# Performance work log

Hardware: AMD Instinct MI355X
Metric: run time of the kernel (lower is better)

Reference implementation:

```python
import jax, jax.numpy as jnp
import numpy as np

N, E, G, D, OUT, VOCAB = 100000, 1600000, 512, 128, 10, 500
BN_EPS = 1e-5


def _lin(h, W, b):
    return h @ W + b


def _mlp(h, W1, b1, W2, b2):
    return _lin(jax.nn.relu(_lin(h, W1, b1)), W2, b2)


def _bn(h, g, b):
    mu = jnp.mean(h, axis=0)
    var = jnp.var(h, axis=0)
    return (h - mu) * jax.lax.rsqrt(var + BN_EPS) * g + b


def setup_inputs() -> dict:
    key = jax.random.key(0)
    ks = jax.random.split(key, 32)
    s = 1.0 / np.sqrt(D)
    inp = {
        'x': jax.random.randint(ks[0], (N,), 0, VOCAB, dtype=jnp.int32),
        'edge_index': jax.random.randint(ks[1], (2, E), 0, N, dtype=jnp.int32),
        'batch': jnp.sort(jax.random.randint(ks[2], (N,), 0, G, dtype=jnp.int32)),
        'emb': jax.random.normal(ks[3], (VOCAB, D), jnp.float32),
        'iw1': jax.random.normal(ks[4], (D, D), jnp.float32) * s,
        'ib1': jnp.zeros((D,), jnp.float32),
        'iw2': jax.random.normal(ks[5], (D, D), jnp.float32) * s,
        'ib2': jnp.zeros((D,), jnp.float32),
        'f1w': jax.random.normal(ks[6], (D, D), jnp.float32) * s,
        'f1b': jnp.zeros((D,), jnp.float32),
        'f2w': jax.random.normal(ks[7], (D, OUT), jnp.float32) * s,
        'f2b': jnp.zeros((OUT,), jnp.float32),
    }
    for i, base in zip(range(3), (8, 14, 20)):
        l = i + 1
        inp[f'c{l}w1'] = jax.random.normal(ks[base], (D, D), jnp.float32) * s
        inp[f'c{l}b1'] = jnp.zeros((D,), jnp.float32)
        inp[f'c{l}w2'] = jax.random.normal(ks[base + 1], (D, D), jnp.float32) * s
        inp[f'c{l}b2'] = jnp.zeros((D,), jnp.float32)
        inp[f'g{l}'] = jnp.ones((D,), jnp.float32)
        inp[f'be{l}'] = jnp.zeros((D,), jnp.float32)
    return inp


def reference(x, edge_index, batch,
              emb, iw1, ib1, iw2, ib2,
              c1w1, c1b1, c1w2, c1b2, g1, be1,
              c2w1, c2b1, c2w2, c2b2, g2, be2,
              c3w1, c3b1, c3w2, c3b2, g3, be3,
              f1w, f1b, f2w, f2b):
    src, dst = edge_index[0], edge_index[1]

    def gin_conv(h, W1, b1, W2, b2):
        # scatter-add neighbor aggregation, eps = 0 -> (1+0)*x + sum_j x_j
        agg = jax.ops.segment_sum(h[src], dst, num_segments=N)
        return _mlp(h + agg, W1, b1, W2, b2)

    h = emb[x]                                   # [N, D] embedding lookup
    h = _mlp(h, iw1, ib1, iw2, ib2)              # initial_mlp
    h = jax.nn.relu(_bn(gin_conv(h, c1w1, c1b1, c1w2, c1b2), g1, be1))
    h = jax.nn.relu(_bn(gin_conv(h, c2w1, c2b1, c2w2, c2b2), g2, be2))
    h = jax.nn.relu(_bn(gin_conv(h, c3w1, c3b1, c3w2, c3b2), g3, be3))
    p = jax.ops.segment_sum(h, batch, num_segments=G)   # global_add_pool [G, D]
    p = jax.nn.relu(_lin(p, f1w, f1b))
    # dropout in eval mode = identity
    return _lin(p, f2w, f2b)                     # [G, OUT]
```

## Files before the change

kernel.cpp:

```cpp
#include <hip/hip_runtime.h>

typedef unsigned short u16;
typedef unsigned int u32;
typedef __bf16 bf16x8 __attribute__((ext_vector_type(8)));
typedef float f32x4 __attribute__((ext_vector_type(4)));

#define MFMA_BF16(a, b, c) __builtin_amdgcn_mfma_f32_16x16x32_bf16(a, b, c, 0, 0, 0)

#define NBUC_MAX 512
#define BCAP 4608
#define EPB 8192

__device__ __forceinline__ float bf2f(u16 h) {
  u32 u = ((u32)h) << 16;
  return __builtin_bit_cast(float, u);
}
__device__ __forceinline__ u16 f2bf(float f) {
  u32 u = __builtin_bit_cast(u32, f);
  u += 0x7fffu + ((u >> 16) & 1u);
  return (u16)(u >> 16);
}

__global__ __launch_bounds__(256) void prep_w6(const float* __restrict__ w0,
                                               const float* __restrict__ w1,
                                               const float* __restrict__ w2,
                                               const float* __restrict__ w3,
                                               const float* __restrict__ w4,
                                               const float* __restrict__ w5,
                                               u16* __restrict__ wt) {
  const int which = blockIdx.x >> 6;
  const float* w = which == 0 ? w0 : which == 1 ? w1 : which == 2 ? w2
                  : which == 3 ? w3 : which == 4 ? w4 : w5;
  int t = (blockIdx.x & 63) * 256 + threadIdx.x;
  int n = t >> 7, k = t & 127;
  wt[which * 16384 + n * 128 + k] = f2bf(w[k * 128 + n]);
}

__global__ __launch_bounds__(128) void mlp0_table(
    const float* __restrict__ emb, const float* __restrict__ w1, const float* __restrict__ b1,
    const float* __restrict__ w2, const float* __restrict__ b2, u16* __restrict__ table) {
  __shared__ float e[128];
  __shared__ float tt[128];
  int r = blockIdx.x, j = threadIdx.x;
  e[j] = emb[r * 128 + j];
  __syncthreads();
  float s = b1[j];
  for (int k = 0; k < 128; ++k) s += e[k] * w1[k * 128 + j];
  tt[j] = s > 0.f ? s : 0.f;
  __syncthreads();
  float s2 = b2[j];
  for (int k = 0; k < 128; ++k) s2 += tt[k] * w2[k * 128 + j];
  table[r * 128 + j] = f2bf(s2);
}

__global__ __launch_bounds__(256) void bucket_scatter(const int* __restrict__ src,
                                                      const int* __restrict__ dst,
                                                      u32* __restrict__ pairs,
                                                      u32* __restrict__ cursor, int E_, int nbuc) {
  __shared__ u32 sv[EPB];
  __shared__ u16 sb[EPB];
  __shared__ u32 lcnt[NBUC_MAX];
  __shared__ u32 lbase[NBUC_MAX];
  const int t = threadIdx.x;
  for (int b = t; b < NBUC_MAX; b += 256) lcnt[b] = 0;
  __syncthreads();
  const int e0 = blockIdx.x * EPB;
#pragma unroll
  for (int it = 0; it < EPB / 256; ++it) {
    int idx = it * 256 + t;
    int e = e0 + idx;
    u32 v = 0u;
    u16 b = 0xffffu;
    if (e < E_) {
      int s = src[e], d = dst[e];
      b = (u16)(d >> 8);
      v = ((u32)s << 8) | (u32)(d & 255);
      atomicAdd(&lcnt[b], 1u);
    }
    sv[idx] = v;
    sb[idx] = b;
  }
  __syncthreads();
  for (int b = t; b < nbuc; b += 256) {
    u32 c = lcnt[b];
    lbase[b] = c ? atomicAdd(&cursor[b], c) : 0u;
    lcnt[b] = 0;
  }
  __syncthreads();
#pragma unroll
  for (int it = 0; it < EPB / 256; ++it) {
    int idx = it * 256 + t;
    u16 b = sb[idx];
    if (b != 0xffffu) {
      u32 r = atomicAdd(&lcnt[b], 1u);
      u32 p = lbase[b] + r;
      if (p < BCAP) pairs[(size_t)b * BCAP + p] = sv[idx];
    }
  }
}

__global__ __launch_bounds__(256) void csr_build(const u32* __restrict__ pairs,
                                                 const u32* __restrict__ cursor,
                                                 u32* __restrict__ csr, int* __restrict__ RS,
                                                 int* __restrict__ DEG, int nrows) {
  __shared__ u32 cnt[256];
  __shared__ u32 offs[256];
  __shared__ u32 basearr[256];
  const int b = blockIdx.x, t = threadIdx.x;
  u32 count = cursor[b];
  if (count > BCAP) count = BCAP;
  cnt[t] = 0;
  __syncthreads();
  const u32* pb = pairs + (size_t)b * BCAP;
  for (u32 i = t; i < count; i += 256) atomicAdd(&cnt[pb[i] & 255u], 1u);
  __syncthreads();
  const u32 my = cnt[t];
  offs[t] = my;
  __syncthreads();
  for (int d = 1; d < 256; d <<= 1) {
    u32 v = (t >= d) ? offs[t - d] : 0u;
    __syncthreads();
    offs[t] += v;
    __syncthreads();
  }
  const u32 excl = offs[t] - my;
  const int node = (b << 8) + t;
  if (node < nrows) {
    RS[node] = b * BCAP + (int)excl;
    DEG[node] = (int)my;
  }
  basearr[t] = excl;
  cnt[t] = 0;
  __syncthreads();
  for (u32 i = t; i < count; i += 256) {
    u32 v = pb[i];
    u32 dl = v & 255u;
    u32 r = atomicAdd(&cnt[dl], 1u);
    csr[(size_t)b * BCAP + basearr[dl] + r] = v >> 8;
  }
}

template <int MODE>
__global__ __launch_bounds__(256) void agg_kernel(
    const u16* __restrict__ Hsrc, const int* __restrict__ x, const u32* __restrict__ csr,
    const int* __restrict__ RS, const int* __restrict__ DEG, const float* __restrict__ scsh,
    u16* __restrict__ AGG, int nrows) {
  int node = blockIdx.x * 4 + (threadIdx.x >> 6);
  if (node >= nrows) return;
  const int lane = threadIdx.x & 63;
  const int grp = lane >> 4;
  const int fl = lane & 15;
  const int deg = DEG[node];
  const u32* cl = csr + RS[node];
  const char* Hb = (const char*)Hsrc;
  const u32 flo = (u32)fl << 4;

  float sc[8], sh[8];
  if (MODE == 1) {
#pragma unroll
    for (int i = 0; i < 8; ++i) {
      sc[i] = scsh[fl * 8 + i];
      sh[i] = scsh[128 + fl * 8 + i];
    }
  }
  float a[8];
#pragma unroll
  for (int i = 0; i < 8; ++i) a[i] = 0.f;

#define ACCUM(vv)                                   \
  {                                                 \
    const u16* p = (const u16*)&(vv);               \
    _Pragma("unroll") for (int i = 0; i < 8; ++i) { \
      float xv = bf2f(p[i]);                        \
      if (MODE == 1) {                              \
        xv = xv * sc[i] + sh[i];                    \
        xv = xv > 0.f ? xv : 0.f;                   \
      }                                             \
      a[i] += xv;                                   \
    }                                               \
  }
#define ROWOFF(idx) ((((u32)(MODE == 0 ? x[(idx)] : (idx))) << 8) + flo)

  if (grp == 0) {
    uint4 v = *(const uint4*)(Hb + ROWOFF(node));
    ACCUM(v);
  }
  int j = grp;
  int cA = (j < deg) ? (int)cl[j] : 0;
  int cB = (j + 4 < deg) ? (int)cl[j + 4] : 0;
  uint4 nv = make_uint4(0u, 0u, 0u, 0u);
  if (j < deg) nv = *(const uint4*)(Hb + ROWOFF(cA));
  while (j < deg) {
    uint4 cv = nv;
    int cn = cB;
    cB = (j + 8 < deg) ? (int)cl[j + 8] : 0;
    if (j + 4 < deg) nv = *(const uint4*)(Hb + ROWOFF(cn));
    ACCUM(cv);
    j += 4;
  }
#undef ROWOFF
#undef ACCUM

#pragma unroll
  for (int i = 0; i < 8; ++i) {
    a[i] += __shfl_xor(a[i], 16);
    a[i] += __shfl_xor(a[i], 32);
  }
  if (grp == 0) {
    u32 o[4];
#pragma unroll
    for (int i = 0; i < 4; ++i) o[i] = (u32)f2bf(a[2 * i]) | ((u32)f2bf(a[2 * i + 1]) << 16);
    *(uint4*)(AGG + (size_t)node * 128 + fl * 8) = *(uint4*)o;
  }
}

__global__ __launch_bounds__(256) void mlp_kernel(
    const u16* __restrict__ X, const u16* __restrict__ W1t, const float* __restrict__ b1,
    const u16* __restrict__ W2t, const float* __restrict__ b2, u16* __restrict__ Y,
    float* __restrict__ stats, int nrows) {
  __shared__ u16 Xs[64 * 136];
  __shared__ u16 Ts[64 * 136];
  const int t = threadIdx.x;
  const int row0 = blockIdx.x * 64;
  {
    const int seg = t & 15;
    const int rb = t >> 4;
#pragma unroll
    for (int p = 0; p < 4; ++p) {
      const int r = rb + p * 16;
      const int gr = row0 + r;
      uint4 v = make_uint4(0u, 0u, 0u, 0u);
      if (gr < nrows) v = *(const uint4*)(X + (size_t)gr * 128 + seg * 8);
      *(uint4*)(Xs + r * 136 + seg * 8) = v;
    }
  }
  __syncthreads();
  const int lane = t & 63;
  const int wave = t >> 6;
  const int n0 = wave * 32;
  const int nl = lane & 15;
  const int quad = lane >> 4;

  bf16x8 bw[2][4];
#pragma unroll
  for (int nt = 0; nt < 2; ++nt)
#pragma unroll
    for (int kk = 0; kk < 4; ++kk)
      bw[nt][kk] = *(const bf16x8*)(W1t + (size_t)(n0 + nt * 16 + nl) * 128 + kk * 32 + quad * 8);

  f32x4 acc[4][2];
#pragma unroll
  for (int mt = 0; mt < 4; ++mt) {
    acc[mt][0] = (f32x4)0.0f;
    acc[mt][1] = (f32x4)0.0f;
  }
#pragma unroll
  for (int kk = 0; kk < 4; ++kk) {
#pragma unroll
    for (int mt = 0; mt < 4; ++mt) {
      bf16x8 a = *(const bf16x8*)(Xs + (mt * 16 + nl) * 136 + kk * 32 + quad * 8);
      acc[mt][0] = MFMA_BF16(a, bw[0][kk], acc[mt][0]);
      acc[mt][1] = MFMA_BF16(a, bw[1][kk], acc[mt][1]);
    }
  }
#pragma unroll
  for (int nt = 0; nt < 2; ++nt) {
    const int n = n0 + nt * 16 + nl;
    const float bias = b1[n];
#pragma unroll
    for (int mt = 0; mt < 4; ++mt)
#pragma unroll
      for (int r = 0; r < 4; ++r) {
        float v = acc[mt][nt][r] + bias;
        v = v > 0.f ? v : 0.f;
        Ts[(mt * 16 + quad * 4 + r) * 136 + n] = f2bf(v);
      }
  }
  __syncthreads();
#pragma unroll
  for (int nt = 0; nt < 2; ++nt)
#pragma unroll
    for (int kk = 0; kk < 4; ++kk)
      bw[nt][kk] = *(const bf16x8*)(W2t + (size_t)(n0 + nt * 16 + nl) * 128 + kk * 32 + quad * 8);
#pragma unroll
  for (int mt = 0; mt < 4; ++mt) {
    acc[mt][0] = (f32x4)0.0f;
    acc[mt][1] = (f32x4)0.0f;
  }
#pragma unroll
  for (int kk = 0; kk < 4; ++kk) {
#pragma unroll
    for (int mt = 0; mt < 4; ++mt) {
      bf16x8 a = *(const bf16x8*)(Ts + (mt * 16 + nl) * 136 + kk * 32 + quad * 8);
      acc[mt][0] = MFMA_BF16(a, bw[0][kk], acc[mt][0]);
      acc[mt][1] = MFMA_BF16(a, bw[1][kk], acc[mt][1]);
    }
  }
  float ssum[2] = {0.f, 0.f}, ssq[2] = {0.f, 0.f};
#pragma unroll
  for (int nt = 0; nt < 2; ++nt) {
    const int n = n0 + nt * 16 + nl;
    const float bias = b2[n];
#pragma unroll
    for (int mt = 0; mt < 4; ++mt)
#pragma unroll
      for (int r = 0; r < 4; ++r) {
        const int row = row0 + mt * 16 + quad * 4 + r;
        float v = acc[mt][nt][r] + bias;
        if (row < nrows) {
          Y[(size_t)row * 128 + n] = f2bf(v);
          ssum[nt] += v;
          ssq[nt] += v * v;
        }
      }
  }
#pragma unroll
  for (int nt = 0; nt < 2; ++nt) {
    float s = ssum[nt], q = ssq[nt];
    s += __shfl_xor(s, 16);
    q += __shfl_xor(q, 16);
    s += __shfl_xor(s, 32);
    q += __shfl_xor(q, 32);
    if (quad == 0) {
      const int n = n0 + nt * 16 + nl;
      atomicAdd(&stats[n], s);
      atomicAdd(&stats[128 + n], q);
    }
  }
}

__global__ __launch_bounds__(128) void bn_finalize(const float* __restrict__ stats,
                                                   const float* __restrict__ g,
                                                   const float* __restrict__ be,
                                                   float* __restrict__ scsh, float invN) {
  int f = threadIdx.x;
  float mu = stats[f] * invN;
  float var = stats[128 + f] * invN - mu * mu;
  float rstd = rsqrtf(var + 1e-5f);
  float sc = rstd * g[f];
  scsh[f] = sc;
  scsh[128 + f] = be[f] - mu * sc;
}

__global__ __launch_bounds__(256) void pool_final(
    const u16* __restrict__ Hh, const int* __restrict__ batch, const float* __restrict__ scsh,
    const float* __restrict__ f1w, const float* __restrict__ f1b, const float* __restrict__ f2w,
    const float* __restrict__ f2b, float* __restrict__ out, int nrows) {
  __shared__ float red[16][128];
  __shared__ float pr[128];
  __shared__ float tt[128];
  const int gid = blockIdx.x, t = threadIdx.x;
  int l = 0, r = nrows;
  while (l < r) {
    int m = (l + r) >> 1;
    if (batch[m] < gid) l = m + 1; else r = m;
  }
  const int s0 = l;
  r = nrows;
  while (l < r) {
    int m = (l + r) >> 1;
    if (batch[m] < gid + 1) l = m + 1; else r = m;
  }
  const int s1 = l;
  const int fl = t & 15;
  const int grp = t >> 4;
  float sc[8], sh[8];
#pragma unroll
  for (int i = 0; i < 8; ++i) {
    sc[i] = scsh[fl * 8 + i];
    sh[i] = scsh[128 + fl * 8 + i];
  }
  float a[8];
#pragma unroll
  for (int i = 0; i < 8; ++i) a[i] = 0.f;
  for (int i = s0 + grp; i < s1; i += 16) {
    uint4 v = *(const uint4*)(Hh + (size_t)i * 128 + fl * 8);
    const u16* pp = (const u16*)&v;
#pragma unroll
    for (int k = 0; k < 8; ++k) {
      float xv = bf2f(pp[k]) * sc[k] + sh[k];
      a[k] += xv > 0.f ? xv : 0.f;
    }
  }
#pragma unroll
  for (int k = 0; k < 8; ++k) red[grp][fl * 8 + k] = a[k];
  __syncthreads();
  if (t < 128) {
    float s = 0.f;
#pragma unroll
    for (int gg2 = 0; gg2 < 16; ++gg2) s += red[gg2][t];
    pr[t] = s;
  }
  __syncthreads();
  if (t < 128) {
    float s = f1b[t];
    for (int k = 0; k < 128; ++k) s += pr[k] * f1w[k * 128 + t];
    tt[t] = s > 0.f ? s : 0.f;
  }
  __syncthreads();
  if (t < 10) {
    float s2 = f2b[t];
    for (int k = 0; k < 128; ++k) s2 += tt[k] * f2w[k * 10 + t];
    out[gid * 10 + t] = s2;
  }
}

extern "C" void kernel_launch(void* const* d_in, const int* in_sizes, int n_in, void* d_out,
                              int out_size, void* d_ws, size_t ws_size, hipStream_t stream) {
  const int* x = (const int*)d_in[0];
  const int* ei = (const int*)d_in[1];
  const int* batch = (const int*)d_in[2];
  const float* emb = (const float*)d_in[3];
  const float* iw1 = (const float*)d_in[4];
  const float* ib1 = (const float*)d_in[5];
  const float* iw2 = (const float*)d_in[6];
  const float* ib2 = (const float*)d_in[7];
  const float* f1w = (const float*)d_in[8];
  const float* f1b = (const float*)d_in[9];
  const float* f2w = (const float*)d_in[10];
  const float* f2b = (const float*)d_in[11];
  const float* cw1[3] = {(const float*)d_in[12], (const float*)d_in[18], (const float*)d_in[24]};
  const float* cb1[3] = {(const float*)d_in[13], (const float*)d_in[19], (const float*)d_in[25]};
  const float* cw2[3] = {(const float*)d_in[14], (const float*)d_in[20], (const float*)d_in[26]};
  const float* cb2[3] = {(const float*)d_in[15], (const float*)d_in[21], (const float*)d_in[27]};
  const float* gg[3] = {(const float*)d_in[16], (const float*)d_in[22], (const float*)d_in[28]};
  const float* bb[3] = {(const float*)d_in[17], (const float*)d_in[23], (const float*)d_in[29]};

  const int N_ = in_sizes[0];
  const int E_ = in_sizes[1] / 2;
  const int V_ = in_sizes[3] / 128;
  const int G_ = out_size / 10;
  const int NBUC = (N_ + 255) >> 8;
  const float invN = 1.0f / (float)N_;

  char* ws = (char*)d_ws;
  u16* H = (u16*)(ws + 0);
  u16* AGG = (u16*)(ws + 25600000);
  u32* PAIRS = (u32*)(ws + 51200000);
  u32* CSR = (u32*)(ws + 60637184);
  int* RS = (int*)(ws + 70074368);
  int* DEG = (int*)(ws + 70474368);
  u32* CUR = (u32*)(ws + 70874368);
  float* STATS = (float*)(ws + 70876416);
  float* SCSH = (float*)(ws + 70879488);
  u16* WT = (u16*)(ws + 70882560);
  u16* TBL = (u16*)(ws + 71079168);

  hipMemsetAsync(ws + 70874368, 0, 5120, stream);

  prep_w6<<<384, 256, 0, stream>>>(cw1[0], cw2[0], cw1[1], cw2[1], cw1[2], cw2[2], WT);
  mlp0_table<<<V_, 128, 0, stream>>>(emb, iw1, ib1, iw2, ib2, TBL);
  bucket_scatter<<<(E_ + EPB - 1) / EPB, 256, 0, stream>>>(ei, ei + E_, PAIRS, CUR, E_, NBUC);
  csr_build<<<NBUC, 256, 0, stream>>>(PAIRS, CUR, CSR, RS, DEG, N_);

  const int ablk = (N_ + 3) / 4;
  const int mblk = (N_ + 63) / 64;
  for (int l = 0; l < 3; ++l) {
    const u16* W1 = WT + (size_t)l * 32768;
    const u16* W2 = WT + (size_t)l * 32768 + 16384;
    if (l == 0)
      agg_kernel<0><<<ablk, 256, 0, stream>>>(TBL, x, CSR, RS, DEG, nullptr, AGG, N_);
    else
      agg_kernel<1><<<ablk, 256, 0, stream>>>(H, nullptr, CSR, RS, DEG, SCSH + (l - 1) * 256,
                                              AGG, N_);
    mlp_kernel<<<mblk, 256, 0, stream>>>(AGG, W1, cb1[l], W2, cb2[l], H, STATS + l * 256, N_);
    bn_finalize<<<1, 128, 0, stream>>>(STATS + l * 256, gg[l], bb[l], SCSH + l * 256, invN);
  }
  pool_final<<<G_, 256, 0, stream>>>(H, batch, SCSH + 2 * 256, f1w, f1b, f2w, f2b,
                                     (float*)d_out, N_);
}
```

Baseline: 543.3 us.

## Unfuse BN-apply from aggregation and drop LDS staging in bucket scatter

Batch-norm scale/shift plus ReLU is moved out of the gather loop into a separate bn_apply kernel that normalizes H in place once per layer, so the aggregation only converts and adds neighbor rows. The aim is to avoid redoing the affine and ReLU for every edge (about 16 times per node). The cost is an extra launch and a full read-write pass over H. Separately, bucket_scatter no longer stages src/dst in shared memory and re-reads them from global memory in the second pass, which frees LDS for higher occupancy at the cost of a second read of the edge list.

New measurement: 570.5 us. +5.0%, slower.

```diff
diff --git a/kernel.cpp b/kernel.cpp
--- a/kernel.cpp
+++ b/kernel.cpp
@@ -57,8 +57,6 @@
                                                       const int* __restrict__ dst,
                                                       u32* __restrict__ pairs,
                                                       u32* __restrict__ cursor, int E_, int nbuc) {
-  __shared__ u32 sv[EPB];
-  __shared__ u16 sb[EPB];
   __shared__ u32 lcnt[NBUC_MAX];
   __shared__ u32 lbase[NBUC_MAX];
   const int t = threadIdx.x;
@@ -67,18 +65,8 @@
   const int e0 = blockIdx.x * EPB;
 #pragma unroll
   for (int it = 0; it < EPB / 256; ++it) {
-    int idx = it * 256 + t;
-    int e = e0 + idx;
-    u32 v = 0u;
-    u16 b = 0xffffu;
-    if (e < E_) {
-      int s = src[e], d = dst[e];
-      b = (u16)(d >> 8);
-      v = ((u32)s << 8) | (u32)(d & 255);
-      atomicAdd(&lcnt[b], 1u);
-    }
-    sv[idx] = v;
-    sb[idx] = b;
+    int e = e0 + it * 256 + t;
+    if (e < E_) atomicAdd(&lcnt[((u32)dst[e]) >> 8], 1u);
   }
   __syncthreads();
   for (int b = t; b < nbuc; b += 256) {
@@ -89,12 +77,13 @@
   __syncthreads();
 #pragma unroll
   for (int it = 0; it < EPB / 256; ++it) {
-    int idx = it * 256 + t;
-    u16 b = sb[idx];
-    if (b != 0xffffu) {
+    int e = e0 + it * 256 + t;
+    if (e < E_) {
+      int d = dst[e];
+      u32 b = ((u32)d) >> 8;
       u32 r = atomicAdd(&lcnt[b], 1u);
       u32 p = lbase[b] + r;
-      if (p < BCAP) pairs[(size_t)b * BCAP + p] = sv[idx];
+      if (p < BCAP) pairs[(size_t)b * BCAP + p] = (((u32)src[e]) << 8) | (u32)(d & 255);
     }
   }
 }
@@ -143,8 +132,7 @@
 template <int MODE>
 __global__ __launch_bounds__(256) void agg_kernel(
     const u16* __restrict__ Hsrc, const int* __restrict__ x, const u32* __restrict__ csr,
-    const int* __restrict__ RS, const int* __restrict__ DEG, const float* __restrict__ scsh,
-    u16* __restrict__ AGG, int nrows) {
+    const int* __restrict__ RS, const int* __restrict__ DEG, u16* __restrict__ AGG, int nrows) {
   int node = blockIdx.x * 4 + (threadIdx.x >> 6);
   if (node >= nrows) return;
   const int lane = threadIdx.x & 63;
@@ -155,14 +143,6 @@
   const char* Hb = (const char*)Hsrc;
   const u32 flo = (u32)fl << 4;
 
-  float sc[8], sh[8];
-  if (MODE == 1) {
-#pragma unroll
-    for (int i = 0; i < 8; ++i) {
-      sc[i] = scsh[fl * 8 + i];
-      sh[i] = scsh[128 + fl * 8 + i];
-    }
-  }
   float a[8];
 #pragma unroll
   for (int i = 0; i < 8; ++i) a[i] = 0.f;
@@ -170,14 +150,7 @@
 #define ACCUM(vv)                                   \
   {                                                 \
     const u16* p = (const u16*)&(vv);               \
-    _Pragma("unroll") for (int i = 0; i < 8; ++i) { \
-      float xv = bf2f(p[i]);                        \
-      if (MODE == 1) {                              \
-        xv = xv * sc[i] + sh[i];                    \
-        xv = xv > 0.f ? xv : 0.f;                   \
-      }                                             \
-      a[i] += xv;                                   \
-    }                                               \
+    _Pragma("unroll") for (int i = 0; i < 8; ++i) a[i] += bf2f(p[i]); \
   }
 #define ROWOFF(idx) ((((u32)(MODE == 0 ? x[(idx)] : (idx))) << 8) + flo)
 
@@ -212,6 +185,24 @@
     for (int i = 0; i < 4; ++i) o[i] = (u32)f2bf(a[2 * i]) | ((u32)f2bf(a[2 * i + 1]) << 16);
     *(uint4*)(AGG + (size_t)node * 128 + fl * 8) = *(uint4*)o;
   }
+}
+
+__global__ __launch_bounds__(256) void bn_apply(u16* __restrict__ Hh,
+                                                const float* __restrict__ scsh, int total16) {
+  int t = blockIdx.x * 256 + threadIdx.x;
+  if (t >= total16) return;
+  int seg = t & 15;
+  uint4 v = *(uint4*)(Hh + (size_t)t * 8);
+  u16* p = (u16*)&v;
+  u16 o[8];
+#pragma unroll
+  for (int i = 0; i < 8; ++i) {
+    int f = seg * 8 + i;
+    float xv = bf2f(p[i]) * scsh[f] + scsh[128 + f];
+    xv = xv > 0.f ? xv : 0.f;
+    o[i] = f2bf(xv);
+  }
+  *(uint4*)(Hh + (size_t)t * 8) = *(uint4*)o;
 }
 
 __global__ __launch_bounds__(256) void mlp_kernel(
@@ -458,11 +449,12 @@
   for (int l = 0; l < 3; ++l) {
     const u16* W1 = WT + (size_t)l * 32768;
     const u16* W2 = WT + (size_t)l * 32768 + 16384;
-    if (l == 0)
-      agg_kernel<0><<<ablk, 256, 0, stream>>>(TBL, x, CSR, RS, DEG, nullptr, AGG, N_);
-    else
-      agg_kernel<1><<<ablk, 256, 0, stream>>>(H, nullptr, CSR, RS, DEG, SCSH + (l - 1) * 256,
-                                              AGG, N_);
+    if (l == 0) {
+      agg_kernel<0><<<ablk, 256, 0, stream>>>(TBL, x, CSR, RS, DEG, AGG, N_);
+    } else {
+      bn_apply<<<(N_ * 16 + 255) / 256, 256, 0, stream>>>(H, SCSH + (l - 1) * 256, N_ * 16);
+      agg_kernel<1><<<ablk, 256, 0, stream>>>(H, nullptr, CSR, RS, DEG, AGG, N_);
+    }
     mlp_kernel<<<mblk, 256, 0, stream>>>(AGG, W1, cb1[l], W2, cb2[l], H, STATS + l * 256, N_);
     bn_finalize<<<1, 128, 0, stream>>>(STATS + l * 256, gg[l], bb[l], SCSH + l * 256, invN);
   }
```
